# Kernel tuning notes

Hardware: AMD Instinct MI355X
Metric: run time of the kernel (lower is better)

Reference implementation:

```python
import jax, jax.numpy as jnp
import numpy as np

N, F, G, E, L, HID, C = 16384, 256, 64, 131072, 3, 512, 2
EPS = 1e-5
IU = F * (F - 1) // 2      # 32640 strict-upper-tri features per graph
IN1 = IU + F * L           # 33408 MLP input width


def setup_inputs() -> dict:
    key = jax.random.key(0)
    ks = jax.random.split(key, 16)

    def w(k, shape, fan_in):
        return jax.random.normal(k, shape, jnp.float32) * (1.0 / np.sqrt(fan_in))

    return {
        "x": jax.random.normal(ks[0], (N, F), jnp.float32),
        "edge_index": jax.random.randint(ks[1], (2, E), 0, N, dtype=jnp.int32),
        "batch": jnp.repeat(jnp.arange(G, dtype=jnp.int32), N // G),  # F nodes per graph
        "lin_src_w": w(ks[2], (L, F, F), F), "lin_src_b": jnp.zeros((L, F), jnp.float32),
        "lin_dst_w": w(ks[3], (L, F, F), F), "lin_dst_b": jnp.zeros((L, F), jnp.float32),
        "att_w": w(ks[4], (L, 2 * F, 1), 2 * F), "att_b": jnp.zeros((L, 1), jnp.float32),
        "bn_g": jnp.ones((IU,), jnp.float32), "bn_b": jnp.zeros((IU,), jnp.float32),
        "bnh_g": jnp.ones((F * L,), jnp.float32), "bnh_b": jnp.zeros((F * L,), jnp.float32),
        "w1": w(ks[5], (IN1, HID), IN1), "b1": jnp.zeros((HID,), jnp.float32),
        "g1": jnp.ones((HID,), jnp.float32), "be1": jnp.zeros((HID,), jnp.float32),
        "w2": w(ks[6], (HID, HID // 2), HID), "b2": jnp.zeros((HID // 2,), jnp.float32),
        "g2": jnp.ones((HID // 2,), jnp.float32), "be2": jnp.zeros((HID // 2,), jnp.float32),
        "w3": w(ks[7], (HID // 2, HID // 2), HID // 2), "b3": jnp.zeros((HID // 2,), jnp.float32),
        "g3": jnp.ones((HID // 2,), jnp.float32), "be3": jnp.zeros((HID // 2,), jnp.float32),
        "w4": w(ks[8], (HID // 2, C), HID // 2), "b4": jnp.zeros((C,), jnp.float32),
    }


def _bn(z, g, b):
    # BatchNorm1d (training-mode batch stats, biased variance, as torch uses for normalization)
    m = jnp.mean(z, 0)
    v = jnp.var(z, 0)
    return (z - m) * jax.lax.rsqrt(v + EPS) * g + b


def _conv(x, src, dst, Ws, bs, Wd, bd, Wa, ba):
    # EdgeLevelAttention layer (heads=1): gather -> concat -> linear -> softmax(heads) -> weighted scatter-add
    x_src = x @ Ws + bs                      # [N, F]
    x_dst = x @ Wd + bd                      # [N, F]
    x_j = x_src[src]                         # [E2, F] source features per edge
    x_i = x_dst[dst]                         # [E2, F] destination features per edge
    alpha = jax.nn.softmax(jnp.concatenate([x_i, x_j], -1) @ Wa + ba, axis=1)  # [E2, 1] (all ones for heads=1)
    msg = x_i * alpha                        # message uses x_i, as in the source
    return jax.ops.segment_sum(msg, dst, num_segments=N)


def reference(x, edge_index, batch, lin_src_w, lin_src_b, lin_dst_w, lin_dst_b,
              att_w, att_b, bn_g, bn_b, bnh_g, bnh_b,
              w1, b1, g1, be1, w2, b2, g2, be2, w3, b3, g3, be3, w4, b4):
    loops = jnp.arange(N, dtype=edge_index.dtype)          # add_self_loops
    src = jnp.concatenate([edge_index[0], loops])
    dst = jnp.concatenate([edge_index[1], loops])

    h = x
    pooled = []
    cnt = jax.ops.segment_sum(jnp.ones((N, 1), x.dtype), batch, num_segments=G)
    for l in range(L):
        h = _conv(h, src, dst, lin_src_w[l], lin_src_b[l],
                  lin_dst_w[l], lin_dst_b[l], att_w[l], att_b[l])
        pooled.append(jax.ops.segment_sum(h, batch, num_segments=G) / cnt)  # global_mean_pool

    iu = np.triu_indices(F, k=1)
    xt = x.reshape(G, F, F)[:, iu[0], iu[1]]               # strict upper triangle per graph [G, IU]
    xt = _bn(xt, bn_g, bn_b)
    hh = _bn(jnp.concatenate(pooled, 1), bnh_g, bnh_b)     # [G, F*L]
    z = jnp.concatenate([xt, hh], 1)                       # [G, IN1]

    z = jax.nn.relu(_bn(z @ w1 + b1, g1, be1))
    z = jax.nn.relu(_bn(z @ w2 + b2, g2, be2))
    z = jax.nn.relu(_bn(z @ w3 + b3, g3, be3))
    return z @ w4 + b4                                     # [G, C]
```

## Files before the change

kernel.cpp:

```cpp
#include <hip/hip_runtime.h>
#include <cstdint>

typedef __attribute__((ext_vector_type(8))) short short8;
typedef __attribute__((ext_vector_type(4))) float f32x4;
typedef unsigned short ushort_t;

static constexpr int NN = 16384, FF = 256, GG = 64, EE = 131072, LL = 3;
static constexpr int HIDN = 512, IU = 32640, IN1 = 33408;
#define EPSV 1e-5f

__device__ inline unsigned short bf16r(float v) {
  unsigned u = __float_as_uint(v);
  u += 0x7FFFu + ((u >> 16) & 1u);
  return (unsigned short)(u >> 16);
}

__global__ __launch_bounds__(256) void k_pre(int* __restrict__ p,
                                             const float* __restrict__ lw,
                                             ushort_t* __restrict__ wh,
                                             ushort_t* __restrict__ wl) {
  int bx = blockIdx.x, t = threadIdx.x;
  if (bx < 65) {
    int i = bx * 256 + t;
    if (i < 16448) p[i] = 0;
  } else {
    int idx = (bx - 65) * 256 + t;
    float v = lw[idx];
    unsigned short h = bf16r(v);
    wh[idx] = h;
    wl[idx] = bf16r(v - __uint_as_float((unsigned)h << 16));
  }
}

__global__ __launch_bounds__(256) void k_hist(const int* __restrict__ dst,
                                              const int* __restrict__ batch,
                                              int* __restrict__ deg, int* __restrict__ cnt) {
  __shared__ int hist[64];
  int bx = blockIdx.x, t = threadIdx.x;
  if (bx < 512) {
    int e = bx * 256 + t;
    atomicAdd(&deg[dst[e]], 1);
  } else {
    if (t < 64) hist[t] = 0;
    __syncthreads();
    int4 v = ((const int4*)batch)[(bx - 512) * 256 + t];
    int a[4] = {v.x, v.y, v.z, v.w};
    int cur = a[0], run = 1;
#pragma unroll
    for (int j = 1; j < 4; ++j) {
      if (a[j] == cur) run++;
      else { atomicAdd(&hist[cur], run); cur = a[j]; run = 1; }
    }
    atomicAdd(&hist[cur], run);
    __syncthreads();
    if (t < 64 && hist[t]) atomicAdd(&cnt[t], hist[t]);
  }
}

template <int SIN>
__global__ __launch_bounds__(256, 3) void k_conv(const void* __restrict__ Ap,
                                                 const ushort_t* __restrict__ Wh3,
                                                 const ushort_t* __restrict__ Wl3,
                                                 const float* __restrict__ bias,
                                                 const int* __restrict__ deg,
                                                 ushort_t* __restrict__ Cb,
                                                 float* __restrict__ pooled_p, int lofs) {
  __shared__ __align__(16) unsigned short Ah[64][72];
  __shared__ __align__(16) unsigned short Bh[128][72], Bl[128][72];
  int n0 = blockIdx.x * 128, m0 = blockIdx.y * 64;
  int t = threadIdx.x;
  int w = t >> 6, l = t & 63;
  int wn = w * 32;
  int lr = l & 15, lg = l >> 4;
  f32x4 acc[4][2];
#pragma unroll
  for (int fm = 0; fm < 4; ++fm)
#pragma unroll
    for (int fn = 0; fn < 2; ++fn) acc[fm][fn] = (f32x4){0.f, 0.f, 0.f, 0.f};

  int am = t >> 2, aq = t & 3;
  int bkp = t & 3, bnf = (t >> 2) & 31, brr = t >> 7;

  for (int ks = 0; ks < 4; ++ks) {
    int k0 = ks * 64;
    if (ks) __syncthreads();
    if (SIN == 0) {
      const float* ap = (const float*)Ap + (size_t)(m0 + am) * FF + k0;
#pragma unroll
      for (int i = 0; i < 4; ++i) {
        int k = aq * 4 + i * 16;
        float4 v = *(const float4*)(ap + k);
        unsigned short h0 = bf16r(v.x), h1 = bf16r(v.y), h2 = bf16r(v.z), h3 = bf16r(v.w);
        *(uint2*)&Ah[am][k] = make_uint2((unsigned)h0 | ((unsigned)h1 << 16),
                                         (unsigned)h2 | ((unsigned)h3 << 16));
      }
    } else {
      const ushort_t* ap = (const ushort_t*)Ap + (size_t)(m0 + am) * FF + k0;
#pragma unroll
      for (int i = 0; i < 4; ++i) {
        int k = aq * 4 + i * 16;
        *(uint2*)&Ah[am][k] = *(const uint2*)(ap + k);
      }
    }
#pragma unroll
    for (int r2 = 0; r2 < 4; ++r2) {
      int k = 2 * bkp + 8 * (brr * 4 + r2);
      const ushort_t* whp = Wh3 + (size_t)(k0 + k) * FF + n0 + bnf * 4;
      const ushort_t* wlp = Wl3 + (size_t)(k0 + k) * FF + n0 + bnf * 4;
      uint2 wha = *(const uint2*)whp;
      uint2 whb = *(const uint2*)(whp + FF);
      uint2 wla = *(const uint2*)wlp;
      uint2 wlb = *(const uint2*)(wlp + FF);
      const ushort_t* pha = (const ushort_t*)&wha;
      const ushort_t* phb = (const ushort_t*)&whb;
      const ushort_t* pla = (const ushort_t*)&wla;
      const ushort_t* plb = (const ushort_t*)&wlb;
#pragma unroll
      for (int j = 0; j < 4; ++j) {
        int n = bnf * 4 + j;
        *(unsigned*)&Bh[n][k] = (unsigned)pha[j] | ((unsigned)phb[j] << 16);
        *(unsigned*)&Bl[n][k] = (unsigned)pla[j] | ((unsigned)plb[j] << 16);
      }
    }
    __syncthreads();
#pragma unroll
    for (int k2 = 0; k2 < 2; ++k2) {
      int kk = k2 * 32 + lg * 8;
      short8 afh[4], bfh[2], bfl[2];
#pragma unroll
      for (int fm = 0; fm < 4; ++fm)
        afh[fm] = *(const short8*)&Ah[fm * 16 + lr][kk];
#pragma unroll
      for (int fn = 0; fn < 2; ++fn) {
        bfh[fn] = *(const short8*)&Bh[wn + fn * 16 + lr][kk];
        bfl[fn] = *(const short8*)&Bl[wn + fn * 16 + lr][kk];
      }
#pragma unroll
      for (int fm = 0; fm < 4; ++fm)
#pragma unroll
        for (int fn = 0; fn < 2; ++fn) {
          acc[fm][fn] = __builtin_amdgcn_mfma_f32_16x16x32_bf16(afh[fm], bfl[fn], acc[fm][fn], 0, 0, 0);
          acc[fm][fn] = __builtin_amdgcn_mfma_f32_16x16x32_bf16(afh[fm], bfh[fn], acc[fm][fn], 0, 0, 0);
        }
    }
  }
  float degf[4][4];
#pragma unroll
  for (int fm = 0; fm < 4; ++fm)
#pragma unroll
    for (int r = 0; r < 4; ++r)
      degf[fm][r] = (float)(deg[m0 + fm * 16 + lg * 4 + r] + 1);
  int g = blockIdx.y >> 2, sub = blockIdx.y & 3;
#pragma unroll
  for (int fn = 0; fn < 2; ++fn) {
    int col = n0 + wn + fn * 16 + lr;
    float bb = bias[col];
    float cs = 0.f;
#pragma unroll
    for (int fm = 0; fm < 4; ++fm) {
      const float* av = (const float*)&acc[fm][fn];
#pragma unroll
      for (int r = 0; r < 4; ++r) {
        int row = m0 + fm * 16 + lg * 4 + r;
        float v = (av[r] + bb) * degf[fm][r];
        cs += v;
        if (Cb) Cb[(size_t)row * FF + col] = bf16r(v);
      }
    }
    cs += __shfl_xor(cs, 16);
    cs += __shfl_xor(cs, 32);
    if (lg == 0)
      pooled_p[((size_t)sub * 64 + g) * (FF * LL) + lofs + col] = cs;
  }
}

__global__ __launch_bounds__(1024, 1) void k_bn_front(const float* __restrict__ x,
                                                      const float* __restrict__ bn_g,
                                                      const float* __restrict__ bn_b,
                                                      const float* __restrict__ pooled_p,
                                                      const int* __restrict__ cnt,
                                                      const float* __restrict__ bnh_g,
                                                      const float* __restrict__ bnh_b,
                                                      ushort_t* __restrict__ zh,
                                                      ushort_t* __restrict__ zl) {
  if (blockIdx.x < 256) {
    __shared__ float sb1[16][256], sb2[16][256];
    __shared__ float rsA[256], bbA[256];
    int i = blockIdx.x, t = threadIdx.x;
    int jq = t & 63, gq = t >> 6;
    int j4 = jq * 4;
    float4 vals[4];
    float s1[4] = {}, s2[4] = {};
#pragma unroll
    for (int r = 0; r < 4; ++r) {
      int g = gq * 4 + r;
      float4 vv = *(const float4*)(x + (size_t)(g * 256 + i) * FF + j4);
      vals[r] = vv;
      s1[0] += vv.x; s2[0] += vv.x * vv.x;
      s1[1] += vv.y; s2[1] += vv.y * vv.y;
      s1[2] += vv.z; s2[2] += vv.z * vv.z;
      s1[3] += vv.w; s2[3] += vv.w * vv.w;
    }
    *(float4*)&sb1[gq][j4] = make_float4(s1[0], s1[1], s1[2], s1[3]);
    *(float4*)&sb2[gq][j4] = make_float4(s2[0], s2[1], s2[2], s2[3]);
    __syncthreads();
    if (t < 256) {
      int j = t;
      float S1 = 0.f, S2 = 0.f;
#pragma unroll
      for (int q = 0; q < 16; ++q) { S1 += sb1[q][j]; S2 += sb2[q][j]; }
      float m = S1 * (1.f / 64.f);
      float var = S2 * (1.f / 64.f) - m * m;
      float rs = 0.f, bb = 0.f;
      if (j > i) {
        int p = i * 255 - (i * (i - 1)) / 2 + (j - i - 1);
        rs = rsqrtf(var + EPSV) * bn_g[p];
        bb = bn_b[p] - m * rs;
      }
      rsA[j] = rs;
      bbA[j] = bb;
    }
    __syncthreads();
    int P0 = i * 255 - (i * (i - 1)) / 2 - i - 1;
#pragma unroll
    for (int r = 0; r < 4; ++r) {
      int g = gq * 4 + r;
      size_t base = (size_t)g * IN1 + P0;
      const float* vf = (const float*)&vals[r];
#pragma unroll
      for (int jj = 0; jj < 4; ++jj) {
        int j = j4 + jj;
        if (j > i) {
          float f = vf[jj] * rsA[j] + bbA[j];
          unsigned short h = bf16r(f);
          zh[base + j] = h;
          zl[base + j] = bf16r(f - __uint_as_float((unsigned)h << 16));
        }
      }
    }
  } else {
    __shared__ float pb1[4][64], pb2[4][64], prs[64], pbb[64];
    int t = threadIdx.x;
    if (t >= 256) return;
    int bx = blockIdx.x - 256;
    int ql = t & 63, gq = t >> 6;
    int q = bx * 64 + ql;
    float vals[16];
    float s1 = 0.f, s2 = 0.f;
#pragma unroll
    for (int gg = 0; gg < 16; ++gg) {
      int g = gq * 16 + gg;
      float v = (pooled_p[((size_t)0 * 64 + g) * (FF * LL) + q] +
                 pooled_p[((size_t)1 * 64 + g) * (FF * LL) + q] +
                 pooled_p[((size_t)2 * 64 + g) * (FF * LL) + q] +
                 pooled_p[((size_t)3 * 64 + g) * (FF * LL) + q]) / (float)cnt[g];
      vals[gg] = v;
      s1 += v;
      s2 += v * v;
    }
    pb1[gq][ql] = s1;
    pb2[gq][ql] = s2;
    __syncthreads();
    if (t < 64) {
      float S1 = pb1[0][t] + pb1[1][t] + pb1[2][t] + pb1[3][t];
      float S2 = pb2[0][t] + pb2[1][t] + pb2[2][t] + pb2[3][t];
      float m = S1 * (1.f / 64.f);
      float var = S2 * (1.f / 64.f) - m * m;
      int qq = bx * 64 + t;
      float rs = rsqrtf(var + EPSV) * bnh_g[qq];
      prs[t] = rs;
      pbb[t] = bnh_b[qq] - m * rs;
    }
    __syncthreads();
#pragma unroll
    for (int gg = 0; gg < 16; ++gg) {
      int g = gq * 16 + gg;
      float f = vals[gg] * prs[ql] + pbb[ql];
      unsigned short h = bf16r(f);
      zh[(size_t)g * IN1 + IU + q] = h;
      zl[(size_t)g * IN1 + IU + q] = bf16r(f - __uint_as_float((unsigned)h << 16));
    }
  }
}

__global__ __launch_bounds__(256, 4) void k_w1(const ushort_t* __restrict__ zh,
                                               const ushort_t* __restrict__ zl,
                                               const float* __restrict__ W,
                                               float* __restrict__ partial) {
  __shared__ __align__(16) unsigned short Zh[64][72], Zl[64][72];
  __shared__ __align__(16) unsigned short Wh[64][72], Wl[64][72];
  int nb = blockIdx.x, s = blockIdx.y;
  int t = threadIdx.x;
  int w = t >> 6, l = t & 63, lr = l & 15, lg = l >> 4;
  int ncol = nb * 64 + w * 16 + lr;
  f32x4 acc[4];
#pragma unroll
  for (int mt = 0; mt < 4; ++mt) acc[mt] = (f32x4){0.f, 0.f, 0.f, 0.f};

  for (int c = s; c < 522; c += 64) {
    int p0 = c * 64;
    if (c != s) __syncthreads();
#pragma unroll
    for (int it = 0; it < 2; ++it) {
      int idx = it * 256 + t;
      int g = idx >> 3, kq = idx & 7;
      *(uint4*)&Zh[g][kq * 8] = *(const uint4*)(zh + (size_t)g * IN1 + p0 + kq * 8);
      *(uint4*)&Zl[g][kq * 8] = *(const uint4*)(zl + (size_t)g * IN1 + p0 + kq * 8);
    }
#pragma unroll
    for (int it = 0; it < 2; ++it) {
      int idx = it * 256 + t;
      int kp = idx >> 4, cg = idx & 15;
      int k = kp * 2;
      const float* wp = W + (size_t)(p0 + k) * HIDN + nb * 64 + cg * 4;
      float4 va = *(const float4*)wp;
      float4 vb = *(const float4*)(wp + HIDN);
      const float* fa = (const float*)&va;
      const float* fb = (const float*)&vb;
#pragma unroll
      for (int j = 0; j < 4; ++j) {
        unsigned ua = __float_as_uint(fa[j]);
        unsigned ub = __float_as_uint(fb[j]);
        unsigned short ha = (unsigned short)(ua >> 16);
        unsigned short hb = (unsigned short)(ub >> 16);
        unsigned short la = bf16r(fa[j] - __uint_as_float(ua & 0xFFFF0000u));
        unsigned short lb = bf16r(fb[j] - __uint_as_float(ub & 0xFFFF0000u));
        int col = cg * 4 + j;
        *(unsigned*)&Wh[col][k] = (unsigned)ha | ((unsigned)hb << 16);
        *(unsigned*)&Wl[col][k] = (unsigned)la | ((unsigned)lb << 16);
      }
    }
    __syncthreads();
#pragma unroll
    for (int k2 = 0; k2 < 2; ++k2) {
      int kloc = k2 * 32 + lg * 8;
      short8 bh = *(const short8*)&Wh[w * 16 + lr][kloc];
      short8 bl = *(const short8*)&Wl[w * 16 + lr][kloc];
#pragma unroll
      for (int mt = 0; mt < 4; ++mt) {
        short8 ah = *(const short8*)&Zh[mt * 16 + lr][kloc];
        short8 al = *(const short8*)&Zl[mt * 16 + lr][kloc];
        acc[mt] = __builtin_amdgcn_mfma_f32_16x16x32_bf16(al, bh, acc[mt], 0, 0, 0);
        acc[mt] = __builtin_amdgcn_mfma_f32_16x16x32_bf16(ah, bl, acc[mt], 0, 0, 0);
        acc[mt] = __builtin_amdgcn_mfma_f32_16x16x32_bf16(ah, bh, acc[mt], 0, 0, 0);
      }
    }
  }
#pragma unroll
  for (int mt = 0; mt < 4; ++mt) {
    const float* av = (const float*)&acc[mt];
#pragma unroll
    for (int r = 0; r < 4; ++r) {
      int g = mt * 16 + lg * 4 + r;
      partial[((size_t)s * 64 + g) * HIDN + ncol] = av[r];
    }
  }
}

__global__ __launch_bounds__(256) void k_reduce(const float* __restrict__ partial,
                                                const float* __restrict__ bias,
                                                float* __restrict__ out, int S, int N) {
  int idx = blockIdx.x * 256 + threadIdx.x;
  if (idx >= 64 * N) return;
  int h = idx % N;
  float a = bias[h];
  for (int s = 0; s < S; ++s) a += partial[(size_t)s * 64 * N + idx];
  out[idx] = a;
}

template <int INBN>
__global__ __launch_bounds__(256, 2) void k_mlp_small(const float* __restrict__ Z,
                                                      const float* __restrict__ ibn_g,
                                                      const float* __restrict__ ibn_b,
                                                      const float* __restrict__ W,
                                                      const float* __restrict__ bias,
                                                      const float* __restrict__ gamma,
                                                      const float* __restrict__ beta,
                                                      float* __restrict__ out, int K, int N) {
  __shared__ float Ws[512 * 16];
  __shared__ float zl[64][132];
  __shared__ float sb1[16][17], sb2[16][17];
  int t = threadIdx.x;
  int h0 = blockIdx.x * 16;
  for (int idx = t; idx < K * 4; idx += 256) {
    int r = idx >> 2, q = idx & 3;
    *(float4*)&Ws[r * 16 + q * 4] = *(const float4*)(W + (size_t)r * N + h0 + q * 4);
  }
  int c = t & 15, gq = t >> 4;
  float acc[4] = {};
  for (int ch = 0; ch < K; ch += 128) {
    for (int idx = t; idx < 64 * 32; idx += 256) {
      int g = idx >> 5, kq = idx & 31;
      *(float4*)&zl[g][kq * 4] = *(const float4*)(Z + (size_t)g * K + ch + kq * 4);
    }
    __syncthreads();
    if (INBN) {
      if (t < 128) {
        float s1 = 0.f, s2 = 0.f;
#pragma unroll
        for (int g = 0; g < 64; ++g) {
          float v = zl[g][t];
          s1 += v;
          s2 += v * v;
        }
        float m = s1 * (1.f / 64.f);
        float var = s2 * (1.f / 64.f) - m * m;
        float rs = rsqrtf(var + EPSV) * ibn_g[ch + t];
        float bb = ibn_b[ch + t] - m * rs;
#pragma unroll
        for (int g = 0; g < 64; ++g)
          zl[g][t] = fmaxf(zl[g][t] * rs + bb, 0.f);
      }
      __syncthreads();
    }
#pragma unroll 8
    for (int kk = 0; kk < 128; ++kk) {
      float w = Ws[(ch + kk) * 16 + c];
#pragma unroll
      for (int i = 0; i < 4; ++i) acc[i] = fmaf(zl[gq * 4 + i][kk], w, acc[i]);
    }
    __syncthreads();
  }
  float bb = bias[h0 + c];
  float s1 = 0.f, s2 = 0.f;
#pragma unroll
  for (int i = 0; i < 4; ++i) {
    acc[i] += bb;
    s1 += acc[i];
    s2 += acc[i] * acc[i];
  }
  sb1[gq][c] = s1;
  sb2[gq][c] = s2;
  __syncthreads();
  float S1 = 0.f, S2 = 0.f;
#pragma unroll
  for (int q = 0; q < 16; ++q) { S1 += sb1[q][c]; S2 += sb2[q][c]; }
  float m = S1 * (1.f / 64.f);
  float var = S2 * (1.f / 64.f) - m * m;
  float rs = rsqrtf(var + EPSV) * gamma[h0 + c];
  float be = beta[h0 + c];
#pragma unroll
  for (int i = 0; i < 4; ++i)
    out[(size_t)(gq * 4 + i) * N + h0 + c] = fmaxf((acc[i] - m) * rs + be, 0.f);
}

__global__ __launch_bounds__(256) void k_final(const float* __restrict__ A,
                                               const float* __restrict__ w4,
                                               const float* __restrict__ b4,
                                               float* __restrict__ out) {
  __shared__ float w4l[512];
  int t = threadIdx.x;
  w4l[t] = w4[t];
  w4l[256 + t] = w4[256 + t];
  __syncthreads();
  int w = t >> 6, l = t & 63;
  for (int g = w * 16; g < w * 16 + 16; ++g) {
    float4 av = *(const float4*)(A + (size_t)g * 256 + l * 4);
    float c0 = av.x * w4l[(l * 4 + 0) * 2] + av.y * w4l[(l * 4 + 1) * 2] +
               av.z * w4l[(l * 4 + 2) * 2] + av.w * w4l[(l * 4 + 3) * 2];
    float c1 = av.x * w4l[(l * 4 + 0) * 2 + 1] + av.y * w4l[(l * 4 + 1) * 2 + 1] +
               av.z * w4l[(l * 4 + 2) * 2 + 1] + av.w * w4l[(l * 4 + 3) * 2 + 1];
#pragma unroll
    for (int o = 32; o > 0; o >>= 1) {
      c0 += __shfl_xor(c0, o);
      c1 += __shfl_xor(c1, o);
    }
    if (l == 0) {
      out[g * 2 + 0] = c0 + b4[0];
      out[g * 2 + 1] = c1 + b4[1];
    }
  }
}

extern "C" void kernel_launch(void* const* d_in, const int* in_sizes, int n_in,
                              void* d_out, int out_size, void* d_ws, size_t ws_size,
                              hipStream_t stream) {
  const float* x = (const float*)d_in[0];
  const int* edge = (const int*)d_in[1];
  const int* batch = (const int*)d_in[2];
  const float* lin_dst_w = (const float*)d_in[5];
  const float* lin_dst_b = (const float*)d_in[6];
  const float* bn_g = (const float*)d_in[9];
  const float* bn_b = (const float*)d_in[10];
  const float* bnh_g = (const float*)d_in[11];
  const float* bnh_b = (const float*)d_in[12];
  const float* w1 = (const float*)d_in[13];
  const float* b1 = (const float*)d_in[14];
  const float* g1 = (const float*)d_in[15];
  const float* be1 = (const float*)d_in[16];
  const float* w2 = (const float*)d_in[17];
  const float* b2 = (const float*)d_in[18];
  const float* g2 = (const float*)d_in[19];
  const float* be2 = (const float*)d_in[20];
  const float* w3 = (const float*)d_in[21];
  const float* b3 = (const float*)d_in[22];
  const float* g3 = (const float*)d_in[23];
  const float* be3 = (const float*)d_in[24];
  const float* w4 = (const float*)d_in[25];
  const float* b4 = (const float*)d_in[26];
  const int* dstp = edge + EE;

  char* ws = (char*)d_ws;
  int* deg = (int*)(ws);
  int* cnt = (int*)(ws + 65536);
  float* bufA = (float*)(ws + 131072);
  float* bufB = (float*)(ws + 131072 + 16777216);
  float* pooled_p = (float*)(ws + 131072 + 2 * 16777216);
  ushort_t* wh3 = (ushort_t*)(ws + 131072 + 2 * 16777216 + 786432);
  ushort_t* wl3 = wh3 + (size_t)LL * FF * FF;
  char* tail = ws + 131072 + 2 * 16777216 + 786432 + 786432;
  float* m1 = (float*)(tail);
  float* m2b = (float*)(tail + 131072);
  float* m3b = (float*)(tail + 131072 + 65536);
  ushort_t* zh = (ushort_t*)bufA;
  ushort_t* zlp = zh + (size_t)64 * IN1;
  float* partial = bufB;
  ushort_t* h1 = (ushort_t*)(ws + 131072 + 16777216);
  ushort_t* h2 = (ushort_t*)(ws + 131072 + 8388608);

  k_pre<<<833, 256, 0, stream>>>(deg, lin_dst_w, wh3, wl3);
  k_hist<<<528, 256, 0, stream>>>(dstp, batch, deg, cnt);

  k_conv<0><<<dim3(2, 256), 256, 0, stream>>>(x, wh3, wl3, lin_dst_b, deg,
                                              h1, pooled_p, 0);
  k_conv<1><<<dim3(2, 256), 256, 0, stream>>>(h1, wh3 + (size_t)FF * FF,
                                              wl3 + (size_t)FF * FF, lin_dst_b + FF, deg,
                                              h2, pooled_p, FF);
  k_conv<1><<<dim3(2, 256), 256, 0, stream>>>(h2, wh3 + (size_t)2 * FF * FF,
                                              wl3 + (size_t)2 * FF * FF, lin_dst_b + 2 * FF,
                                              deg, (ushort_t*)nullptr, pooled_p, 2 * FF);

  k_bn_front<<<268, 1024, 0, stream>>>(x, bn_g, bn_b, pooled_p, cnt, bnh_g, bnh_b, zh, zlp);

  k_w1<<<dim3(8, 64), 256, 0, stream>>>(zh, zlp, w1, partial);
  k_reduce<<<128, 256, 0, stream>>>(partial, b1, m1, 64, HIDN);

  k_mlp_small<1><<<16, 256, 0, stream>>>(m1, g1, be1, w2, b2, g2, be2, m2b, HIDN, 256);
  k_mlp_small<0><<<16, 256, 0, stream>>>(m2b, nullptr, nullptr, w3, b3, g3, be3, m3b, 256, 256);

  k_final<<<1, 256, 0, stream>>>(m3b, w4, b4, (float*)d_out);
}
```

Baseline: 178.3 us.

## Replace split-K partial buffer with atomics, fold final layer into MLP kernel

The W1 GEMM now accumulates its split-K results with atomicAdd straight into a zeroed m1 buffer, which removes the partial buffer and the separate reduce kernel. Biases b1/b2/b3 are dropped because the batch norm that follows cancels them. The last linear layer is fused into the second small-MLP kernel through shuffle reductions and atomics into the output, which removes k_final and saves two launches in total. This costs extra atomic traffic on m1 and makes the floating-point summation order nondeterministic.

```diff
diff --git a/kernel.cpp b/kernel.cpp
--- a/kernel.cpp
+++ b/kernel.cpp
@@ -16,6 +16,8 @@
 }
 
 __global__ __launch_bounds__(256) void k_pre(int* __restrict__ p,
+                                             float* __restrict__ m1,
+                                             float* __restrict__ outf,
                                              const float* __restrict__ lw,
                                              ushort_t* __restrict__ wh,
                                              ushort_t* __restrict__ wl) {
@@ -23,8 +25,12 @@
   if (bx < 65) {
     int i = bx * 256 + t;
     if (i < 16448) p[i] = 0;
+  } else if (bx < 193) {
+    m1[(bx - 65) * 256 + t] = 0.f;
+  } else if (bx == 193) {
+    if (t < 128) outf[t] = 0.f;
   } else {
-    int idx = (bx - 65) * 256 + t;
+    int idx = (bx - 194) * 256 + t;
     float v = lw[idx];
     unsigned short h = bf16r(v);
     wh[idx] = h;
@@ -286,7 +292,7 @@
 __global__ __launch_bounds__(256, 4) void k_w1(const ushort_t* __restrict__ zh,
                                                const ushort_t* __restrict__ zl,
                                                const float* __restrict__ W,
-                                               float* __restrict__ partial) {
+                                               float* __restrict__ m1) {
   __shared__ __align__(16) unsigned short Zh[64][72], Zl[64][72];
   __shared__ __align__(16) unsigned short Wh[64][72], Wl[64][72];
   int nb = blockIdx.x, s = blockIdx.y;
@@ -352,30 +358,20 @@
 #pragma unroll
     for (int r = 0; r < 4; ++r) {
       int g = mt * 16 + lg * 4 + r;
-      partial[((size_t)s * 64 + g) * HIDN + ncol] = av[r];
-    }
-  }
-}
-
-__global__ __launch_bounds__(256) void k_reduce(const float* __restrict__ partial,
-                                                const float* __restrict__ bias,
-                                                float* __restrict__ out, int S, int N) {
-  int idx = blockIdx.x * 256 + threadIdx.x;
-  if (idx >= 64 * N) return;
-  int h = idx % N;
-  float a = bias[h];
-  for (int s = 0; s < S; ++s) a += partial[(size_t)s * 64 * N + idx];
-  out[idx] = a;
-}
-
-template <int INBN>
+      atomicAdd(&m1[(size_t)g * HIDN + ncol], av[r]);
+    }
+  }
+}
+
+template <int INBN, int FIN>
 __global__ __launch_bounds__(256, 2) void k_mlp_small(const float* __restrict__ Z,
                                                       const float* __restrict__ ibn_g,
                                                       const float* __restrict__ ibn_b,
                                                       const float* __restrict__ W,
-                                                      const float* __restrict__ bias,
                                                       const float* __restrict__ gamma,
                                                       const float* __restrict__ beta,
+                                                      const float* __restrict__ w4,
+                                                      const float* __restrict__ b4,
                                                       float* __restrict__ out, int K, int N) {
   __shared__ float Ws[512 * 16];
   __shared__ float zl[64][132];
@@ -421,11 +417,9 @@
     }
     __syncthreads();
   }
-  float bb = bias[h0 + c];
   float s1 = 0.f, s2 = 0.f;
 #pragma unroll
   for (int i = 0; i < 4; ++i) {
-    acc[i] += bb;
     s1 += acc[i];
     s2 += acc[i] * acc[i];
   }
@@ -439,36 +433,36 @@
   float var = S2 * (1.f / 64.f) - m * m;
   float rs = rsqrtf(var + EPSV) * gamma[h0 + c];
   float be = beta[h0 + c];
-#pragma unroll
-  for (int i = 0; i < 4; ++i)
-    out[(size_t)(gq * 4 + i) * N + h0 + c] = fmaxf((acc[i] - m) * rs + be, 0.f);
-}
-
-__global__ __launch_bounds__(256) void k_final(const float* __restrict__ A,
-                                               const float* __restrict__ w4,
-                                               const float* __restrict__ b4,
-                                               float* __restrict__ out) {
-  __shared__ float w4l[512];
-  int t = threadIdx.x;
-  w4l[t] = w4[t];
-  w4l[256 + t] = w4[256 + t];
-  __syncthreads();
-  int w = t >> 6, l = t & 63;
-  for (int g = w * 16; g < w * 16 + 16; ++g) {
-    float4 av = *(const float4*)(A + (size_t)g * 256 + l * 4);
-    float c0 = av.x * w4l[(l * 4 + 0) * 2] + av.y * w4l[(l * 4 + 1) * 2] +
-               av.z * w4l[(l * 4 + 2) * 2] + av.w * w4l[(l * 4 + 3) * 2];
-    float c1 = av.x * w4l[(l * 4 + 0) * 2 + 1] + av.y * w4l[(l * 4 + 1) * 2 + 1] +
-               av.z * w4l[(l * 4 + 2) * 2 + 1] + av.w * w4l[(l * 4 + 3) * 2 + 1];
-#pragma unroll
-    for (int o = 32; o > 0; o >>= 1) {
-      c0 += __shfl_xor(c0, o);
-      c1 += __shfl_xor(c1, o);
-    }
-    if (l == 0) {
-      out[g * 2 + 0] = c0 + b4[0];
-      out[g * 2 + 1] = c1 + b4[1];
-    }
+  if (!FIN) {
+#pragma unroll
+    for (int i = 0; i < 4; ++i)
+      out[(size_t)(gq * 4 + i) * N + h0 + c] = fmaxf((acc[i] - m) * rs + be, 0.f);
+  } else {
+    float wa = w4[(h0 + c) * 2 + 0], wb = w4[(h0 + c) * 2 + 1];
+    float ca[4], cb[4];
+#pragma unroll
+    for (int i = 0; i < 4; ++i) {
+      float v = fmaxf((acc[i] - m) * rs + be, 0.f);
+      ca[i] = v * wa;
+      cb[i] = v * wb;
+    }
+#pragma unroll
+    for (int o = 1; o < 16; o <<= 1) {
+#pragma unroll
+      for (int i = 0; i < 4; ++i) {
+        ca[i] += __shfl_xor(ca[i], o);
+        cb[i] += __shfl_xor(cb[i], o);
+      }
+    }
+    if (c == 0) {
+#pragma unroll
+      for (int i = 0; i < 4; ++i) {
+        int g = gq * 4 + i;
+        atomicAdd(&out[g * 2 + 0], ca[i]);
+        atomicAdd(&out[g * 2 + 1], cb[i]);
+      }
+    }
+    if (blockIdx.x == 0 && t < 128) atomicAdd(&out[t], b4[t & 1]);
   }
 }
 
@@ -485,15 +479,12 @@
   const float* bnh_g = (const float*)d_in[11];
   const float* bnh_b = (const float*)d_in[12];
   const float* w1 = (const float*)d_in[13];
-  const float* b1 = (const float*)d_in[14];
   const float* g1 = (const float*)d_in[15];
   const float* be1 = (const float*)d_in[16];
   const float* w2 = (const float*)d_in[17];
-  const float* b2 = (const float*)d_in[18];
   const float* g2 = (const float*)d_in[19];
   const float* be2 = (const float*)d_in[20];
   const float* w3 = (const float*)d_in[21];
-  const float* b3 = (const float*)d_in[22];
   const float* g3 = (const float*)d_in[23];
   const float* be3 = (const float*)d_in[24];
   const float* w4 = (const float*)d_in[25];
@@ -504,21 +495,19 @@
   int* deg = (int*)(ws);
   int* cnt = (int*)(ws + 65536);
   float* bufA = (float*)(ws + 131072);
-  float* bufB = (float*)(ws + 131072 + 16777216);
   float* pooled_p = (float*)(ws + 131072 + 2 * 16777216);
   ushort_t* wh3 = (ushort_t*)(ws + 131072 + 2 * 16777216 + 786432);
   ushort_t* wl3 = wh3 + (size_t)LL * FF * FF;
   char* tail = ws + 131072 + 2 * 16777216 + 786432 + 786432;
   float* m1 = (float*)(tail);
   float* m2b = (float*)(tail + 131072);
-  float* m3b = (float*)(tail + 131072 + 65536);
   ushort_t* zh = (ushort_t*)bufA;
   ushort_t* zlp = zh + (size_t)64 * IN1;
-  float* partial = bufB;
   ushort_t* h1 = (ushort_t*)(ws + 131072 + 16777216);
   ushort_t* h2 = (ushort_t*)(ws + 131072 + 8388608);
-
-  k_pre<<<833, 256, 0, stream>>>(deg, lin_dst_w, wh3, wl3);
+  float* outf = (float*)d_out;
+
+  k_pre<<<962, 256, 0, stream>>>(deg, m1, outf, lin_dst_w, wh3, wl3);
   k_hist<<<528, 256, 0, stream>>>(dstp, batch, deg, cnt);
 
   k_conv<0><<<dim3(2, 256), 256, 0, stream>>>(x, wh3, wl3, lin_dst_b, deg,
@@ -532,11 +521,9 @@
 
   k_bn_front<<<268, 1024, 0, stream>>>(x, bn_g, bn_b, pooled_p, cnt, bnh_g, bnh_b, zh, zlp);
 
-  k_w1<<<dim3(8, 64), 256, 0, stream>>>(zh, zlp, w1, partial);
-  k_reduce<<<128, 256, 0, stream>>>(partial, b1, m1, 64, HIDN);
-
-  k_mlp_small<1><<<16, 256, 0, stream>>>(m1, g1, be1, w2, b2, g2, be2, m2b, HIDN, 256);
-  k_mlp_small<0><<<16, 256, 0, stream>>>(m2b, nullptr, nullptr, w3, b3, g3, be3, m3b, 256, 256);
-
-  k_final<<<1, 256, 0, stream>>>(m3b, w4, b4, (float*)d_out);
-}
+  k_w1<<<dim3(8, 64), 256, 0, stream>>>(zh, zlp, w1, m1);
+  k_mlp_small<1, 0><<<16, 256, 0, stream>>>(m1, g1, be1, w2, g2, be2,
+                                            nullptr, nullptr, m2b, HIDN, 256);
+  k_mlp_small<0, 1><<<16, 256, 0, stream>>>(m2b, nullptr, nullptr, w3, g3, be3,
+                                            w4, b4, outf, 256, 256);
+}
```

New measurement: 156.7 us (median of 2 runs). 12.1% less time.
